# Performance work log

Measured on AMD Instinct MI355X. Metric: run time of the kernel, lower is better.

The kernel has to match this reference:

```python
import jax, jax.numpy as jnp
import numpy as np

EPS = 1e-6  # flax.linen.LayerNorm default

def layer_norm(x, scale, bias):
    mean = jnp.mean(x, axis=-1, keepdims=True)
    var = jnp.mean(jnp.square(x - mean), axis=-1, keepdims=True)
    return (x - mean) * jax.lax.rsqrt(var + EPS) * scale + bias

def setup_inputs() -> dict:
    key = jax.random.key(0)
    ks = jax.random.split(key, 4)
    B, P, D, H = 2, 2048, 768, 12
    hd = D // H
    x = jax.random.normal(ks[0], (B, P, D), dtype=jnp.float32)
    W_qkv = jax.random.normal(ks[1], (D, 3 * D), dtype=jnp.float32) * (D ** -0.5)
    W_out = jax.random.normal(ks[2], (D, D), dtype=jnp.float32) * (D ** -0.5)
    b_out = jnp.zeros((D,), dtype=jnp.float32)
    return {
        "x": x,
        "W_qkv": W_qkv,
        "q_scale": jnp.ones((hd,), jnp.float32),
        "q_bias": jnp.zeros((hd,), jnp.float32),
        "k_scale": jnp.ones((hd,), jnp.float32),
        "k_bias": jnp.zeros((hd,), jnp.float32),
        "o_scale": jnp.ones((D,), jnp.float32),
        "o_bias": jnp.zeros((D,), jnp.float32),
        "W_out": W_out,
        "b_out": b_out,
    }

def reference(x, W_qkv, q_scale, q_bias, k_scale, k_bias, o_scale, o_bias, W_out, b_out):
    B, P, D = x.shape
    H = 12
    hd = D // H
    scale = hd ** -0.5
    # fused QKV projection, no bias
    qkv = (x @ W_qkv).reshape(B, P, 3, H, hd).transpose(2, 0, 3, 1, 4)  # [3,B,H,P,hd]
    q, k, v = qkv[0], qkv[1], qkv[2]
    # per-head QK LayerNorm over head_dim
    q = layer_norm(q, q_scale, q_bias) * scale
    k = layer_norm(k, k_scale, k_bias)
    attn = jnp.einsum("bhqd,bhkd->bhqk", q, k)
    attn = jax.nn.softmax(attn, axis=-1)
    out = jnp.einsum("bhqk,bhkd->bhqd", attn, v)  # [B,H,P,hd]
    out = jnp.swapaxes(out, 1, 2).reshape(B, P, D)
    out = layer_norm(out, o_scale, o_bias)
    return out @ W_out + b_out
```

## Files before the change

kernel.cpp:

```cpp
#include <hip/hip_runtime.h>
#include <hip/hip_bf16.h>

#define B_  2
#define P_  2048
#define D_  768
#define H_  12
#define HD_ 64
#define M_  (B_ * P_)
#define N1_ (3 * D_)

typedef __attribute__((ext_vector_type(8))) short short8;
typedef __attribute__((ext_vector_type(4))) float f32x4;
typedef __attribute__((ext_vector_type(16))) float f32x16;
typedef unsigned short ushort;

__device__ __forceinline__ ushort f2bf(float f) {
    unsigned u = __float_as_uint(f);
    u += 0x7fffu + ((u >> 16) & 1u);
    return (ushort)(u >> 16);
}

__global__ __launch_bounds__(512) void gemm_qkv_mfma(
        const float* __restrict__ x, const float* __restrict__ w,
        const float* __restrict__ qs, const float* __restrict__ qb,
        const float* __restrict__ ks, const float* __restrict__ kb,
        ushort* __restrict__ qkv) {
    __shared__ __align__(16) ushort As[128][40];
    __shared__ __align__(16) ushort Bs[128][40];

    const int tid  = threadIdx.x;
    const int lane = tid & 63;
    const int wv   = tid >> 6;
    const int quad = lane >> 4;
    const int col  = lane & 15;
    const int wr   = (wv >> 1) * 32;
    const int wc   = (wv & 1) * 64;
    const int rowBase = blockIdx.y * 128;
    const int colBase = blockIdx.x * 128;

    const int am0 = tid >> 3, ac4 = tid & 7;
    const int nB  = tid & 127, kq = tid >> 7;

    float4 apre[2];
    float  bpre[8];
    auto load_tile = [&](int kt) {
        const int k0 = kt * 32;
        apre[0] = *(const float4*)(x + (size_t)(rowBase + am0) * D_ + k0 + ac4 * 4);
        apre[1] = *(const float4*)(x + (size_t)(rowBase + am0 + 64) * D_ + k0 + ac4 * 4);
#pragma unroll
        for (int j = 0; j < 8; j++)
            bpre[j] = w[(size_t)(k0 + kq * 8 + j) * N1_ + colBase + nB];
    };

    f32x4 acc[2][4];
#pragma unroll
    for (int i = 0; i < 2; i++)
#pragma unroll
        for (int j = 0; j < 4; j++) acc[i][j] = (f32x4){0.f, 0.f, 0.f, 0.f};

    load_tile(0);
    const int NT = D_ / 32;
    for (int kt = 0; kt < NT; kt++) {
        __syncthreads();
        {
            ushort u0[4] = {f2bf(apre[0].x), f2bf(apre[0].y), f2bf(apre[0].z), f2bf(apre[0].w)};
            ushort u1[4] = {f2bf(apre[1].x), f2bf(apre[1].y), f2bf(apre[1].z), f2bf(apre[1].w)};
            *(uint2*)&As[am0][ac4 * 4]      = *(uint2*)u0;
            *(uint2*)&As[am0 + 64][ac4 * 4] = *(uint2*)u1;
            ushort us[8];
#pragma unroll
            for (int j = 0; j < 8; j++) us[j] = f2bf(bpre[j]);
            *(short8*)&Bs[nB][kq * 8] = *(short8*)&us[0];
        }
        __syncthreads();
        if (kt + 1 < NT) load_tile(kt + 1);

        short8 af[2], bf[4];
#pragma unroll
        for (int mt = 0; mt < 2; mt++) af[mt] = *(const short8*)&As[wr + mt * 16 + col][quad * 8];
#pragma unroll
        for (int nt = 0; nt < 4; nt++) bf[nt] = *(const short8*)&Bs[wc + nt * 16 + col][quad * 8];
#pragma unroll
        for (int mt = 0; mt < 2; mt++)
#pragma unroll
            for (int nt = 0; nt < 4; nt++)
                acc[mt][nt] = __builtin_amdgcn_mfma_f32_16x16x32_bf16(af[mt], bf[nt], acc[mt][nt], 0, 0, 0);
    }

    const int comp = colBase / D_;
    const int rem  = colBase + wc - comp * D_;
    const int h    = rem >> 6;
    float sc4[4] = {0, 0, 0, 0}, bi4[4] = {0, 0, 0, 0};
    if (comp == 0) {
#pragma unroll
        for (int nt = 0; nt < 4; nt++) { sc4[nt] = qs[nt * 16 + col]; bi4[nt] = qb[nt * 16 + col]; }
    } else if (comp == 1) {
#pragma unroll
        for (int nt = 0; nt < 4; nt++) { sc4[nt] = ks[nt * 16 + col]; bi4[nt] = kb[nt * 16 + col]; }
    }

#pragma unroll
    for (int mt = 0; mt < 2; mt++) {
#pragma unroll
        for (int r = 0; r < 4; r++) {
            int m  = rowBase + wr + mt * 16 + quad * 4 + r;
            int bb = m >> 11;
            int p  = m & 2047;
            float v0 = acc[mt][0][r], v1 = acc[mt][1][r], v2 = acc[mt][2][r], v3 = acc[mt][3][r];
            if (comp < 2) {
                float s = v0 + v1 + v2 + v3;
#pragma unroll
                for (int off = 1; off < 16; off <<= 1) s += __shfl_xor(s, off, 64);
                float mean = s * (1.0f / 64.0f);
                float d0 = v0 - mean, d1 = v1 - mean, d2 = v2 - mean, d3 = v3 - mean;
                float sq = d0 * d0 + d1 * d1 + d2 * d2 + d3 * d3;
#pragma unroll
                for (int off = 1; off < 16; off <<= 1) sq += __shfl_xor(sq, off, 64);
                float inv = rsqrtf(sq * (1.0f / 64.0f) + 1e-6f);
                v0 = d0 * inv * sc4[0] + bi4[0];
                v1 = d1 * inv * sc4[1] + bi4[1];
                v2 = d2 * inv * sc4[2] + bi4[2];
                v3 = d3 * inv * sc4[3] + bi4[3];
                if (comp == 0) { v0 *= 0.125f; v1 *= 0.125f; v2 *= 0.125f; v3 *= 0.125f; }
            }
            size_t base = ((((size_t)comp * B_ + bb) * H_ + h) * P_ + p) * HD_;
            qkv[base +  0 + col] = f2bf(v0);
            qkv[base + 16 + col] = f2bf(v1);
            qkv[base + 32 + col] = f2bf(v2);
            qkv[base + 48 + col] = f2bf(v3);
        }
    }
}

__global__ __launch_bounds__(256) void attn_split(const ushort* __restrict__ qkv,
                                                  float* __restrict__ o0,
                                                  float* __restrict__ o1,
                                                  float* __restrict__ l0,
                                                  float* __restrict__ l1) {
    const int p0 = blockIdx.x * 128;
    const int bh = blockIdx.y;
    const int s  = blockIdx.z;
    const int b  = bh / H_, h = bh % H_;
    float* opart = s ? o1 : o0;
    float* lpart = s ? l1 : l0;
    const int tid  = threadIdx.x;
    const int lane = tid & 63;
    const int wv   = tid >> 6;
    const int half = lane >> 5;
    const int n32  = lane & 31;

    __shared__ __align__(16) ushort Ks[64][72];
    __shared__ __align__(16) ushort Vs[64][72];
    __shared__ __align__(16) ushort Ps[4][32][72];

    const size_t hs = (size_t)P_ * HD_;
    const ushort* qg = qkv + ((size_t)(0 * B_ + b) * H_ + h) * hs + (size_t)(p0 + wv * 32) * HD_;
    const ushort* kg = qkv + ((size_t)(1 * B_ + b) * H_ + h) * hs + (size_t)s * (P_ / 2) * HD_;
    const ushort* vg = qkv + ((size_t)(2 * B_ + b) * H_ + h) * hs + (size_t)s * (P_ / 2) * HD_;

    short8 aq[4];
#pragma unroll
    for (int ks2 = 0; ks2 < 4; ks2++)
        aq[ks2] = *(const short8*)(qg + (size_t)n32 * HD_ + ks2 * 16 + half * 8);

    float lrow[16];
#pragma unroll
    for (int r = 0; r < 16; r++) lrow[r] = 0.f;
    f32x16 oacc[2];
#pragma unroll
    for (int nt = 0; nt < 2; nt++)
#pragma unroll
        for (int r = 0; r < 16; r++) oacc[nt][r] = 0.f;

    const int kr = tid >> 3, kc8 = tid & 7;
    const int vd = tid & 63,  vkh = tid >> 6;

    uint4  kpre[2];
    ushort vpre[16];
    auto load_tile = [&](int kt) {
        const ushort* kg_t = kg + (size_t)kt * 64 * HD_;
        const ushort* vg_t = vg + (size_t)kt * 64 * HD_;
        kpre[0] = *(const uint4*)(kg_t + (size_t)kr * HD_ + kc8 * 8);
        kpre[1] = *(const uint4*)(kg_t + (size_t)(kr + 32) * HD_ + kc8 * 8);
#pragma unroll
        for (int j = 0; j < 16; j++)
            vpre[j] = vg_t[(size_t)(vkh * 16 + j) * HD_ + vd];
    };

    load_tile(0);
    const int NT = (P_ / 2) / 64;
    for (int kt = 0; kt < NT; kt++) {
        __syncthreads();
        *(uint4*)&Ks[kr][kc8 * 8]      = kpre[0];
        *(uint4*)&Ks[kr + 32][kc8 * 8] = kpre[1];
        *(short8*)&Vs[vd][vkh * 16]     = *(short8*)&vpre[0];
        *(short8*)&Vs[vd][vkh * 16 + 8] = *(short8*)&vpre[8];
        __syncthreads();
        if (kt + 1 < NT) load_tile(kt + 1);

        f32x16 sc[2];
#pragma unroll
        for (int nt = 0; nt < 2; nt++) {
#pragma unroll
            for (int r = 0; r < 16; r++) sc[nt][r] = 0.f;
#pragma unroll
            for (int ks2 = 0; ks2 < 4; ks2++) {
                short8 kb2 = *(const short8*)&Ks[nt * 32 + n32][ks2 * 16 + half * 8];
                sc[nt] = __builtin_amdgcn_mfma_f32_32x32x16_bf16(aq[ks2], kb2, sc[nt], 0, 0, 0);
            }
        }

#pragma unroll
        for (int reg = 0; reg < 16; reg++) {
            int row = (reg & 3) + 8 * (reg >> 2) + 4 * half;
#pragma unroll
            for (int nt = 0; nt < 2; nt++) {
                float p = __expf(fminf(sc[nt][reg], 60.f));
                lrow[reg] += p;
                Ps[wv][row][nt * 32 + n32] = f2bf(p);
            }
        }

#pragma unroll
        for (int kp = 0; kp < 4; kp++) {
            short8 pa = *(const short8*)&Ps[wv][n32][kp * 16 + half * 8];
#pragma unroll
            for (int nt = 0; nt < 2; nt++) {
                short8 vb = *(const short8*)&Vs[nt * 32 + n32][kp * 16 + half * 8];
                oacc[nt] = __builtin_amdgcn_mfma_f32_32x32x16_bf16(pa, vb, oacc[nt], 0, 0, 0);
            }
        }
    }

#pragma unroll
    for (int reg = 0; reg < 16; reg++) {
#pragma unroll
        for (int off = 1; off < 32; off <<= 1)
            lrow[reg] += __shfl_xor(lrow[reg], off, 64);
    }

    if (n32 == 0) {
#pragma unroll
        for (int reg = 0; reg < 16; reg++) {
            int row = (reg & 3) + 8 * (reg >> 2) + 4 * half;
            lpart[(size_t)bh * P_ + p0 + wv * 32 + row] = lrow[reg];
        }
    }

    float* Psf = (float*)&Ps[wv][0][0];
#pragma unroll
    for (int nt = 0; nt < 2; nt++) {
#pragma unroll
        for (int reg = 0; reg < 16; reg++) {
            int row = (reg & 3) + 8 * (reg >> 2) + 4 * half;
            Psf[row * 36 + n32] = oacc[nt][reg];
        }
#pragma unroll
        for (int i = 0; i < 4; i++) {
            int ql = i * 8 + (lane >> 3);
            int c4 = lane & 7;
            float4 v = *(const float4*)&Psf[ql * 36 + c4 * 4];
            *(float4*)(opart + ((size_t)bh * P_ + p0 + wv * 32 + ql) * HD_ + nt * 32 + c4 * 4) = v;
        }
    }
}

__global__ __launch_bounds__(256) void ln_o(const float* __restrict__ o0,
                                            const float* __restrict__ o1,
                                            const float* __restrict__ l0,
                                            const float* __restrict__ l1,
                                            ushort* __restrict__ lnb,
                                            const float* __restrict__ osc,
                                            const float* __restrict__ ob) {
    __shared__ float red[4];
    __shared__ float red2[4];
    const int row = blockIdx.x;
    const int b   = row >> 11;
    const int p   = row & (P_ - 1);
    const int tid = threadIdx.x;

    auto src = [&](int d) {
        int h = d >> 6;
        size_t lr  = (size_t)(b * H_ + h) * P_ + p;
        size_t idx = lr * HD_ + (d & 63);
        return (o0[idx] + o1[idx]) / (l0[lr] + l1[lr]);
    };
    float v0 = src(tid);
    float v1 = src(tid + 256);
    float v2 = src(tid + 512);
    float s = v0 + v1 + v2;
#pragma unroll
    for (int o = 32; o > 0; o >>= 1) s += __shfl_xor(s, o, 64);
    if ((tid & 63) == 0) red[tid >> 6] = s;
    __syncthreads();
    float mean = (red[0] + red[1] + red[2] + red[3]) * (1.0f / 768.0f);
    float d0 = v0 - mean, d1 = v1 - mean, d2 = v2 - mean;
    float sq = d0 * d0 + d1 * d1 + d2 * d2;
#pragma unroll
    for (int o = 32; o > 0; o >>= 1) sq += __shfl_xor(sq, o, 64);
    if ((tid & 63) == 0) red2[tid >> 6] = sq;
    __syncthreads();
    float var = (red2[0] + red2[1] + red2[2] + red2[3]) * (1.0f / 768.0f);
    float inv = rsqrtf(var + 1e-6f);
    const size_t base = (size_t)row * D_;
    lnb[base + tid]       = f2bf(d0 * inv * osc[tid]       + ob[tid]);
    lnb[base + tid + 256] = f2bf(d1 * inv * osc[tid + 256] + ob[tid + 256]);
    lnb[base + tid + 512] = f2bf(d2 * inv * osc[tid + 512] + ob[tid + 512]);
}

__global__ __launch_bounds__(256) void gemm_out_mfma(
        const ushort* __restrict__ a, const float* __restrict__ w,
        const float* __restrict__ bias, float* __restrict__ out) {
    __shared__ __align__(16) ushort As[64][40];
    __shared__ __align__(16) ushort Bs[64][40];

    const int tid  = threadIdx.x;
    const int lane = tid & 63;
    const int wv   = tid >> 6;
    const int quad = lane >> 4;
    const int col  = lane & 15;
    const int wr   = (wv >> 1) * 32;
    const int wc   = (wv & 1) * 32;
    const int rowBase = blockIdx.y * 64;
    const int colBase = blockIdx.x * 64;

    const int am  = tid >> 2, ac8 = tid & 3;
    const int nB  = tid & 63, kq = tid >> 6;

    uint4 apre;
    float bpre[8];
    auto load_tile = [&](int kt) {
        const int k0 = kt * 32;
        apre = *(const uint4*)(a + (size_t)(rowBase + am) * D_ + k0 + ac8 * 8);
#pragma unroll
        for (int j = 0; j < 8; j++)
            bpre[j] = w[(size_t)(k0 + kq * 8 + j) * D_ + colBase + nB];
    };

    f32x4 acc[2][2];
#pragma unroll
    for (int i = 0; i < 2; i++)
#pragma unroll
        for (int j = 0; j < 2; j++) acc[i][j] = (f32x4){0.f, 0.f, 0.f, 0.f};

    load_tile(0);
    const int NT = D_ / 32;
    for (int kt = 0; kt < NT; kt++) {
        __syncthreads();
        *(uint4*)&As[am][ac8 * 8] = apre;
        {
            ushort us[8];
#pragma unroll
            for (int j = 0; j < 8; j++) us[j] = f2bf(bpre[j]);
            *(short8*)&Bs[nB][kq * 8] = *(short8*)&us[0];
        }
        __syncthreads();
        if (kt + 1 < NT) load_tile(kt + 1);

        short8 af[2], bf[2];
#pragma unroll
        for (int mt = 0; mt < 2; mt++) af[mt] = *(const short8*)&As[wr + mt * 16 + col][quad * 8];
#pragma unroll
        for (int nt = 0; nt < 2; nt++) bf[nt] = *(const short8*)&Bs[wc + nt * 16 + col][quad * 8];
#pragma unroll
        for (int mt = 0; mt < 2; mt++)
#pragma unroll
            for (int nt = 0; nt < 2; nt++)
                acc[mt][nt] = __builtin_amdgcn_mfma_f32_16x16x32_bf16(af[mt], bf[nt], acc[mt][nt], 0, 0, 0);
    }

    float b2[2];
#pragma unroll
    for (int nt = 0; nt < 2; nt++) b2[nt] = bias[colBase + wc + nt * 16 + col];
#pragma unroll
    for (int mt = 0; mt < 2; mt++) {
#pragma unroll
        for (int r = 0; r < 4; r++) {
            int m = rowBase + wr + mt * 16 + quad * 4 + r;
            float* dst = out + (size_t)m * D_ + colBase + wc;
#pragma unroll
            for (int nt = 0; nt < 2; nt++)
                dst[nt * 16 + col] = acc[mt][nt][r] + b2[nt];
        }
    }
}

extern "C" void kernel_launch(void* const* d_in, const int* in_sizes, int n_in,
                              void* d_out, int out_size, void* d_ws, size_t ws_size,
                              hipStream_t stream) {
    const float* x    = (const float*)d_in[0];
    const float* Wqkv = (const float*)d_in[1];
    const float* qs   = (const float*)d_in[2];
    const float* qb   = (const float*)d_in[3];
    const float* ks   = (const float*)d_in[4];
    const float* kb   = (const float*)d_in[5];
    const float* osc  = (const float*)d_in[6];
    const float* ob   = (const float*)d_in[7];
    const float* Wout = (const float*)d_in[8];
    const float* bout = (const float*)d_in[9];
    float* out = (float*)d_out;

    ushort* qkv    = (ushort*)d_ws;
    float*  opart0 = (float*)(qkv + (size_t)3 * B_ * H_ * P_ * HD_);
    float*  l0     = opart0 + (size_t)B_ * H_ * P_ * HD_;
    float*  l1     = l0 + (size_t)B_ * H_ * P_;
    float*  opart1 = out;
    ushort* ln_buf = qkv;

    gemm_qkv_mfma<<<dim3(N1_ / 128, M_ / 128), 512, 0, stream>>>(x, Wqkv, qs, qb, ks, kb, qkv);
    attn_split<<<dim3(P_ / 128, B_ * H_, 2), 256, 0, stream>>>(qkv, opart0, opart1, l0, l1);
    ln_o<<<dim3(M_), 256, 0, stream>>>(opart0, opart1, l0, l1, ln_buf, osc, ob);
    gemm_out_mfma<<<dim3(D_ / 64, M_ / 64), 256, 0, stream>>>(ln_buf, Wout, bout, out);
}
```

Measured before the change: 208.0 us.

## Pre-convert GEMM operands to bf16 and use exp2 softmax with folded log2e scale

```diff
diff --git a/kernel.cpp b/kernel.cpp
--- a/kernel.cpp
+++ b/kernel.cpp
@@ -20,8 +20,20 @@
     return (ushort)(u >> 16);
 }
 
+#define QSCALE 0.1803368801111243f
+
+__global__ __launch_bounds__(256) void cvt_bf16(const float* __restrict__ src,
+                                                ushort* __restrict__ dst, int n4) {
+    int i = blockIdx.x * 256 + threadIdx.x;
+    if (i < n4) {
+        float4 v = *(const float4*)(src + (size_t)i * 4);
+        ushort u4[4] = {f2bf(v.x), f2bf(v.y), f2bf(v.z), f2bf(v.w)};
+        *(uint2*)(dst + (size_t)i * 4) = *(uint2*)u4;
+    }
+}
+
 __global__ __launch_bounds__(512) void gemm_qkv_mfma(
-        const float* __restrict__ x, const float* __restrict__ w,
+        const ushort* __restrict__ x, const ushort* __restrict__ w,
         const float* __restrict__ qs, const float* __restrict__ qb,
         const float* __restrict__ ks, const float* __restrict__ kb,
         ushort* __restrict__ qkv) {
@@ -38,15 +50,14 @@
     const int rowBase = blockIdx.y * 128;
     const int colBase = blockIdx.x * 128;
 
-    const int am0 = tid >> 3, ac4 = tid & 7;
+    const int amr = tid >> 2, ac8 = tid & 3;
     const int nB  = tid & 127, kq = tid >> 7;
 
-    float4 apre[2];
-    float  bpre[8];
+    uint4  apre;
+    ushort bpre[8];
     auto load_tile = [&](int kt) {
         const int k0 = kt * 32;
-        apre[0] = *(const float4*)(x + (size_t)(rowBase + am0) * D_ + k0 + ac4 * 4);
-        apre[1] = *(const float4*)(x + (size_t)(rowBase + am0 + 64) * D_ + k0 + ac4 * 4);
+        apre = *(const uint4*)(x + (size_t)(rowBase + amr) * D_ + k0 + ac8 * 8);
 #pragma unroll
         for (int j = 0; j < 8; j++)
             bpre[j] = w[(size_t)(k0 + kq * 8 + j) * N1_ + colBase + nB];
@@ -62,16 +73,8 @@
     const int NT = D_ / 32;
     for (int kt = 0; kt < NT; kt++) {
         __syncthreads();
-        {
-            ushort u0[4] = {f2bf(apre[0].x), f2bf(apre[0].y), f2bf(apre[0].z), f2bf(apre[0].w)};
-            ushort u1[4] = {f2bf(apre[1].x), f2bf(apre[1].y), f2bf(apre[1].z), f2bf(apre[1].w)};
-            *(uint2*)&As[am0][ac4 * 4]      = *(uint2*)u0;
-            *(uint2*)&As[am0 + 64][ac4 * 4] = *(uint2*)u1;
-            ushort us[8];
-#pragma unroll
-            for (int j = 0; j < 8; j++) us[j] = f2bf(bpre[j]);
-            *(short8*)&Bs[nB][kq * 8] = *(short8*)&us[0];
-        }
+        *(uint4*)&As[amr][ac8 * 8] = apre;
+        *(short8*)&Bs[nB][kq * 8]  = *(short8*)&bpre[0];
         __syncthreads();
         if (kt + 1 < NT) load_tile(kt + 1);
 
@@ -121,7 +124,7 @@
                 v1 = d1 * inv * sc4[1] + bi4[1];
                 v2 = d2 * inv * sc4[2] + bi4[2];
                 v3 = d3 * inv * sc4[3] + bi4[3];
-                if (comp == 0) { v0 *= 0.125f; v1 *= 0.125f; v2 *= 0.125f; v3 *= 0.125f; }
+                if (comp == 0) { v0 *= QSCALE; v1 *= QSCALE; v2 *= QSCALE; v3 *= QSCALE; }
             }
             size_t base = ((((size_t)comp * B_ + bb) * H_ + h) * P_ + p) * HD_;
             qkv[base +  0 + col] = f2bf(v0);
@@ -215,9 +218,10 @@
             int row = (reg & 3) + 8 * (reg >> 2) + 4 * half;
 #pragma unroll
             for (int nt = 0; nt < 2; nt++) {
-                float p = __expf(fminf(sc[nt][reg], 60.f));
-                lrow[reg] += p;
-                Ps[wv][row][nt * 32 + n32] = f2bf(p);
+                float p = exp2f(fminf(sc[nt][reg], 86.f));
+                unsigned u = __float_as_uint(p);
+                lrow[reg] += __uint_as_float(u & 0xffff0000u);
+                Ps[wv][row][nt * 32 + n32] = (ushort)(u >> 16);
             }
         }
 
@@ -309,7 +313,7 @@
 }
 
 __global__ __launch_bounds__(256) void gemm_out_mfma(
-        const ushort* __restrict__ a, const float* __restrict__ w,
+        const ushort* __restrict__ a, const ushort* __restrict__ w,
         const float* __restrict__ bias, float* __restrict__ out) {
     __shared__ __align__(16) ushort As[64][40];
     __shared__ __align__(16) ushort Bs[64][40];
@@ -327,8 +331,8 @@
     const int am  = tid >> 2, ac8 = tid & 3;
     const int nB  = tid & 63, kq = tid >> 6;
 
-    uint4 apre;
-    float bpre[8];
+    uint4  apre;
+    ushort bpre[8];
     auto load_tile = [&](int kt) {
         const int k0 = kt * 32;
         apre = *(const uint4*)(a + (size_t)(rowBase + am) * D_ + k0 + ac8 * 8);
@@ -348,12 +352,7 @@
     for (int kt = 0; kt < NT; kt++) {
         __syncthreads();
         *(uint4*)&As[am][ac8 * 8] = apre;
-        {
-            ushort us[8];
-#pragma unroll
-            for (int j = 0; j < 8; j++) us[j] = f2bf(bpre[j]);
-            *(short8*)&Bs[nB][kq * 8] = *(short8*)&us[0];
-        }
+        *(short8*)&Bs[nB][kq * 8] = *(short8*)&bpre[0];
         __syncthreads();
         if (kt + 1 < NT) load_tile(kt + 1);
 
@@ -401,14 +400,21 @@
     float* out = (float*)d_out;
 
     ushort* qkv    = (ushort*)d_ws;
-    float*  opart0 = (float*)(qkv + (size_t)3 * B_ * H_ * P_ * HD_);
-    float*  l0     = opart0 + (size_t)B_ * H_ * P_ * HD_;
-    float*  l1     = l0 + (size_t)B_ * H_ * P_;
+    float*  opart0 = (float*)(qkv + 9437184);
+    float*  l0     = opart0 + 3145728;
+    float*  l1     = l0 + 49152;
+    ushort* wob    = (ushort*)(l1 + 49152);
+    ushort* xb     = (ushort*)opart0;
+    ushort* wqb    = xb + 3145728;
     float*  opart1 = out;
     ushort* ln_buf = qkv;
 
-    gemm_qkv_mfma<<<dim3(N1_ / 128, M_ / 128), 512, 0, stream>>>(x, Wqkv, qs, qb, ks, kb, qkv);
+    cvt_bf16<<<dim3(786432 / 256), 256, 0, stream>>>(x, xb, 786432);
+    cvt_bf16<<<dim3(442368 / 256), 256, 0, stream>>>(Wqkv, wqb, 442368);
+    cvt_bf16<<<dim3(147456 / 256), 256, 0, stream>>>(Wout, wob, 147456);
+
+    gemm_qkv_mfma<<<dim3(N1_ / 128, M_ / 128), 512, 0, stream>>>(xb, wqb, qs, qb, ks, kb, qkv);
     attn_split<<<dim3(P_ / 128, B_ * H_, 2), 256, 0, stream>>>(qkv, opart0, opart1, l0, l1);
     ln_o<<<dim3(M_), 256, 0, stream>>>(opart0, opart1, l0, l1, ln_buf, osc, ob);
-    gemm_out_mfma<<<dim3(D_ / 64, M_ / 64), 256, 0, stream>>>(ln_buf, Wout, bout, out);
-}
+    gemm_out_mfma<<<dim3(D_ / 64, M_ / 64), 256, 0, stream>>>(ln_buf, wob, bout, out);
+}
```

Measured after the change: 254.7 us. 22.4% more time.
